# Performance work log

Hardware: AMD Instinct MI355X
Metric: run time of the kernel (lower is better)

The kernel has to match this reference:

```python
import jax, jax.numpy as jnp
import numpy as np

T, A, E, N, W, HID, FD = 4096, 1024, 512, 32768, 10, 150, 20
GI = 2 * A + E  # 2560
BINS = jnp.array([1, 2, 3, 4, 8, 16, 32, 64], dtype=jnp.int32)


def _mlp(x, W1, b1, W2, b2, W3, b3):
    # Score module: Linear->ReLU->Linear->ReLU->Linear->1 (dropout is a no-op in eval)
    h = jax.nn.relu(x @ W1 + b1)
    h = jax.nn.relu(h @ W2 + b2)
    return h @ W3 + b3


def setup_inputs() -> dict:
    key = jax.random.key(0)
    ks = jax.random.split(key, 20)
    s = 0.02
    inp = {
        "states": jax.random.normal(ks[0], (T, A), jnp.float32),
        "embeds": jax.random.normal(ks[1], (T, E), jnp.float32),
        "span_starts": jax.random.randint(ks[2], (N,), 0, T - W, jnp.int32),
        "span_widths": jax.random.randint(ks[3], (N,), 1, W + 1, jnp.int32),
        # attention Score params (input A)
        "Wa1": jax.random.normal(ks[4], (A, HID)) * s, "ba1": jnp.zeros((HID,)),
        "Wa2": jax.random.normal(ks[5], (HID, HID)) * s, "ba2": jnp.zeros((HID,)),
        "Wa3": jax.random.normal(ks[6], (HID, 1)) * s, "ba3": jnp.zeros((1,)),
        # width Feature embedding table: len(bins)+1 = 9 rows
        "width_emb": jax.random.normal(ks[7], (9, FD)) * s,
        # mention Score params (input GI + FD)
        "Ws1": jax.random.normal(ks[8], (GI + FD, HID)) * s, "bs1": jnp.zeros((HID,)),
        "Ws2": jax.random.normal(ks[9], (HID, HID)) * s, "bs2": jnp.zeros((HID,)),
        "Ws3": jax.random.normal(ks[10], (HID, 1)) * s, "bs3": jnp.zeros((1,)),
    }
    return inp


def reference(states, embeds, span_starts, span_widths,
              Wa1, ba1, Wa2, ba2, Wa3, ba3, width_emb,
              Ws1, bs1, Ws2, bs2, Ws3, bs3):
    # per-token attention logits  [T]
    attns = _mlp(states, Wa1, ba1, Wa2, ba2, Wa3, ba3).squeeze(-1)
    offs = jnp.arange(W)                                   # [W]
    pos = span_starts[:, None] + offs[None, :]             # [N, W]
    mask = offs[None, :] < span_widths[:, None]            # ragged span mask
    pos_c = jnp.clip(pos, 0, T - 1)
    logit = jnp.where(mask, attns[pos_c], -jnp.inf)        # [N, W]
    w = jax.nn.softmax(logit, axis=1)                      # per-span softmax
    attn_sum = jnp.einsum('nw,nwe->ne', w, embeds[pos_c])  # [N, E]
    ends = span_starts + span_widths - 1
    bin_idx = jnp.sum(span_widths[:, None] >= BINS[None, :], axis=1)
    size = width_emb[bin_idx]                              # [N, FD]
    g = jnp.concatenate([states[span_starts], states[ends], attn_sum, size], axis=1)
    scores = _mlp(g, Ws1, bs1, Ws2, bs2, Ws3, bs3).squeeze(-1)  # [N]
    return scores
```

## Files before the change

kernel.cpp:

```cpp
#include <hip/hip_runtime.h>
#include <math.h>

#define T_TOK 4096
#define A_DIM 1024
#define E_DIM 512
#define N_SPAN 32768
#define W_MAX 10
#define HID 150
#define FD 20

#define PR  160
#define KP2 160

#define WS_ATTNS 0
#define WS_PB    4096
#define WS_WPACK 1314816
#define WS_SB    1627856
#define WS_EB    3725008
#define PB_P0 0
#define PB_P1 655360
#define PB_P2 1310720
#define PB_P3 1966080
#define WP_ST  0
#define WP_V   491520
#define WP_A2  573440
#define WP_S2  599040
#define WP_WE1 624640
#define WP_TOTAL 626080
#define SB_PIECES 524288
#define EB_PIECES 262144
#define PK_ITEMS (WP_TOTAL + SB_PIECES + EB_PIECES)

typedef short  bf16x8 __attribute__((ext_vector_type(8)));
typedef float  f32x4  __attribute__((ext_vector_type(4)));

__device__ __forceinline__ float4 ld4(const float* p) { return *(const float4*)p; }

__device__ __forceinline__ unsigned short f2bf(float f) {
    unsigned u = __float_as_uint(f);
    unsigned r = u + 0x7fffu + ((u >> 16) & 1u);
    return (unsigned short)(r >> 16);
}
__device__ __forceinline__ float bf2f(short s) {
    return __uint_as_float(((unsigned)(unsigned short)s) << 16);
}
__device__ __forceinline__ bf16x8 cvt_frag(const float* p) {
    float4 u = ld4(p), v = ld4(p + 4);
    bf16x8 f;
    f[0] = (short)f2bf(u.x); f[1] = (short)f2bf(u.y);
    f[2] = (short)f2bf(u.z); f[3] = (short)f2bf(u.w);
    f[4] = (short)f2bf(v.x); f[5] = (short)f2bf(v.y);
    f[6] = (short)f2bf(v.z); f[7] = (short)f2bf(v.w);
    return f;
}

typedef const __attribute__((address_space(1))) unsigned int as1_u32;
typedef __attribute__((address_space(3))) unsigned int as3_u32;
__device__ __forceinline__ void dma16(const void* g, void* l) {
    __builtin_amdgcn_global_load_lds((as1_u32*)g, (as3_u32*)l, 16, 0, 0);
}
template<int N> __device__ __forceinline__ void waitv() {
    asm volatile("s_waitcnt vmcnt(%0)" :: "n"(N) : "memory");
}

__global__ __launch_bounds__(256) void prepack_kernel(
    const float* __restrict__ states, const float* __restrict__ embeds,
    const float* __restrict__ Wa1, const float* __restrict__ Ws1,
    const float* __restrict__ Wa2, const float* __restrict__ Ws2,
    const float* __restrict__ width_emb,
    unsigned short* __restrict__ wp, unsigned short* __restrict__ Sb,
    unsigned short* __restrict__ Eb)
{
    int idx = blockIdx.x * 256 + threadIdx.x;
    if (idx >= PK_ITEMS) return;
    if (idx < WP_TOTAL) {
        float v = 0.f;
        if (idx < WP_V) {
            int gidx = idx / 163840, r = idx % 163840;
            int ngrp = r / 81920, r2 = r % 81920;
            int c = r2 / 2560, d = r2 % 2560;
            int n = d >> 5, qsw = (d >> 3) & 3, off = d & 7;
            int q = qsw ^ ((n >> 1) & 3);
            int k = c * 32 + q * 8 + off;
            int gn = ngrp * 80 + n;
            const float* W = (gidx == 0) ? Wa1 : Ws1 + (size_t)(gidx - 1) * 1024 * HID;
            if (gn < HID) v = W[(size_t)k * HID + gn];
        } else if (idx < WP_A2) {
            int r = idx - WP_V;
            int ngrp = r / 40960, r2 = r % 40960;
            int c = r2 / 2560, d = r2 % 2560;
            int n = d >> 5, qsw = (d >> 3) & 3, off = d & 7;
            int q = qsw ^ ((n >> 1) & 3);
            int k = c * 32 + q * 8 + off;
            int gn = ngrp * 80 + n;
            if (gn < HID) v = Ws1[(size_t)(2048 + k) * HID + gn];
        } else if (idx < WP_S2) {
            int e = idx - WP_A2;
            int n = e / KP2, k = e % KP2;
            if (n < HID && k < HID) v = Wa2[(size_t)k * HID + n];
        } else if (idx < WP_WE1) {
            int e = idx - WP_S2;
            int n = e / KP2, k = e % KP2;
            if (n < HID && k < HID) v = Ws2[(size_t)k * HID + n];
        } else {
            int e = idx - WP_WE1;
            int b = e / KP2, n = e % KP2;
            if (n < HID)
                for (int k = 0; k < FD; ++k)
                    v = fmaf(width_emb[b * FD + k], Ws1[(size_t)(2560 + k) * HID + n], v);
        }
        wp[idx] = f2bf(v);
    } else if (idx < WP_TOTAL + SB_PIECES) {
        int p = idx - WP_TOTAL;
        int mb = p >> 11, r = p & 2047;
        int c = r >> 6, d8 = r & 63;
        int m = d8 >> 2, qsw = d8 & 3;
        int q = qsw ^ ((m >> 1) & 3);
        const float* src = states + (size_t)(mb * 16 + m) * A_DIM + c * 32 + q * 8;
        *(bf16x8*)(Sb + (size_t)p * 8) = cvt_frag(src);
    } else {
        int p = idx - WP_TOTAL - SB_PIECES;
        int mb = p >> 10, r = p & 1023;
        int c = r >> 6, d8 = r & 63;
        int m = d8 >> 2, qsw = d8 & 3;
        int q = qsw ^ ((m >> 1) & 3);
        const float* src = embeds + (size_t)(mb * 16 + m) * E_DIM + c * 32 + q * 8;
        *(bf16x8*)(Eb + (size_t)p * 8) = cvt_frag(src);
    }
}

template<int NC>
__device__ __forceinline__ void gemm_dma(
    const unsigned short* __restrict__ srcA, const unsigned short* __restrict__ srcB,
    unsigned short (*__restrict__ bufB)[2560], unsigned short (*__restrict__ bufA)[512],
    int lane, int l15, int quad, f32x4 (&acc)[5])
{
    const int swz = (quad ^ ((l15 >> 1) & 3)) * 8;
    const int bl = l15 * 32 + swz;
#define DMAC(c) { _Pragma("unroll")                                          \
        for (int i = 0; i < 5; ++i)                                          \
            dma16(srcB + (size_t)(c) * 2560 + i * 512 + lane * 8,            \
                  &bufB[(c) % 3][i * 512]);                                  \
        dma16(srcA + (size_t)(c) * 512 + lane * 8, &bufA[(c) % 3][0]); }
    DMAC(0);
    DMAC(1);
#pragma unroll
    for (int c = 0; c < NC; ++c) {
        if (c + 2 < NC) DMAC(c + 2);
        if (c + 2 < NC)      waitv<12>();
        else if (c + 1 < NC) waitv<6>();
        else                 waitv<0>();
        bf16x8 af = *(const bf16x8*)(&bufA[c % 3][0] + bl);
        const unsigned short* bb = &bufB[c % 3][0];
#pragma unroll
        for (int t = 0; t < 5; ++t) {
            bf16x8 bf = *(const bf16x8*)(bb + t * 512 + bl);
            acc[t] = __builtin_amdgcn_mfma_f32_16x16x32_bf16(af, bf, acc[t], 0, 0, 0);
        }
    }
#undef DMAC
}

__global__ __launch_bounds__(64) void token_kernel(
    const unsigned short* __restrict__ Sb, const unsigned short* __restrict__ Eb,
    const unsigned short* __restrict__ wp, unsigned short* __restrict__ Pb)
{
    __shared__ __align__(16) unsigned short bufB[3][2560];
    __shared__ __align__(16) unsigned short bufA[3][512];

    const int lane = threadIdx.x, l15 = lane & 15, quad = lane >> 4;
    const int task = blockIdx.x;

    f32x4 acc[5];
#pragma unroll
    for (int t = 0; t < 5; ++t)
#pragma unroll
        for (int i = 0; i < 4; ++i) acc[t][i] = 0.f;

    int m0, gidx, ngrp;
    if (task < 1536) {
        const int mb = task / 6;
        m0 = mb * 16;
        const int sub = task % 6;
        gidx = sub >> 1;
        ngrp = sub & 1;
        const unsigned short* srcA = Sb + (size_t)mb * 16384;
        const unsigned short* srcB = wp + WP_ST + gidx * 163840 + ngrp * 81920;
        gemm_dma<32>(srcA, srcB, bufB, bufA, lane, l15, quad, acc);
    } else {
        const int e = task - 1536;
        const int mb = e >> 1;
        m0 = mb * 16;
        ngrp = e & 1;
        gidx = 3;
        const unsigned short* srcA = Eb + (size_t)mb * 8192;
        const unsigned short* srcB = wp + WP_V + ngrp * 40960;
        gemm_dma<16>(srcA, srcB, bufB, bufA, lane, l15, quad, acc);
    }

    unsigned short* Pg = Pb + (size_t)gidx * 655360;
#pragma unroll
    for (int t = 0; t < 5; ++t) {
        const int col = ngrp * 80 + t * 16 + l15;
#pragma unroll
        for (int i = 0; i < 4; ++i)
            Pg[(size_t)(m0 + quad * 4 + i) * PR + col] =
                (col < HID) ? f2bf(acc[t][i]) : (unsigned short)0;
    }
}

__global__ __launch_bounds__(64) void attn_tail_kernel(
    const unsigned short* __restrict__ P0, const float* __restrict__ ba1,
    const unsigned short* __restrict__ wp, const float* __restrict__ ba2,
    const float* __restrict__ Wa3, const float* __restrict__ ba3,
    float* __restrict__ attns)
{
    const int t0 = blockIdx.x * 16;
    const int lane = threadIdx.x, l15 = lane & 15, quad = lane >> 4;

    f32x4 acc[10];
#pragma unroll
    for (int nt = 0; nt < 10; ++nt)
#pragma unroll
        for (int i = 0; i < 4; ++i) acc[nt][i] = 0.f;

    const unsigned short* prow = P0 + (size_t)(t0 + l15) * PR;
    const unsigned short* bb = wp + WP_A2 + l15 * KP2 + quad * 8;

#pragma unroll
    for (int c = 0; c < 5; ++c) {
        const int k0 = c * 32;
        const int kk = k0 + quad * 8;
        bf16x8 raw = *(const bf16x8*)(prow + kk);
        bf16x8 af;
#pragma unroll
        for (int j = 0; j < 8; ++j) {
            const float b = (kk + j < HID) ? ba1[kk + j] : 0.f;
            af[j] = (short)f2bf(fmaxf(bf2f(raw[j]) + b, 0.f));
        }
#pragma unroll
        for (int nt = 0; nt < 10; ++nt) {
            bf16x8 bf = *(const bf16x8*)(bb + nt * 16 * KP2 + k0);
            acc[nt] = __builtin_amdgcn_mfma_f32_16x16x32_bf16(af, bf, acc[nt], 0, 0, 0);
        }
    }

    float sc[4] = {0.f, 0.f, 0.f, 0.f};
#pragma unroll
    for (int nt = 0; nt < 10; ++nt) {
        const int col = nt * 16 + l15;
        const float w3 = (col < HID) ? Wa3[col] : 0.f;
        const float b2 = (col < HID) ? ba2[col] : 0.f;
#pragma unroll
        for (int i = 0; i < 4; ++i)
            sc[i] = fmaf(fmaxf(acc[nt][i] + b2, 0.f), w3, sc[i]);
    }
#pragma unroll
    for (int off = 8; off >= 1; off >>= 1)
#pragma unroll
        for (int i = 0; i < 4; ++i) sc[i] += __shfl_down(sc[i], off, 16);
    if (l15 == 0) {
        const float b3 = ba3[0];
#pragma unroll
        for (int i = 0; i < 4; ++i) attns[t0 + quad * 4 + i] = sc[i] + b3;
    }
}

__global__ __launch_bounds__(256) void span_kernel(
    const unsigned short* __restrict__ Pb, const float* __restrict__ attns,
    const unsigned short* __restrict__ wp,
    const int* __restrict__ span_starts, const int* __restrict__ span_widths,
    const float* __restrict__ bs1, const float* __restrict__ bs2,
    const float* __restrict__ Ws3, const float* __restrict__ bs3,
    float* __restrict__ out)
{
    __shared__ unsigned short sHb[32][168];
    __shared__ float s_wgt[32][W_MAX];
    __shared__ int s_st[32], s_wd[32], s_bin[32];
    __shared__ float sPart[4][32];
    __shared__ float sb1[KP2];

    const int tid = threadIdx.x;
    const int n0s = blockIdx.x * 32;

    if (tid < KP2) sb1[tid] = (tid < HID) ? bs1[tid] : 0.f;
    if (tid < 32) {
        int st = span_starts[n0s + tid], wd = span_widths[n0s + tid];
        s_st[tid] = st; s_wd[tid] = wd;
        s_bin[tid] = (wd >= 1) + (wd >= 2) + (wd >= 3) + (wd >= 4) +
                     (wd >= 8) + (wd >= 16) + (wd >= 32) + (wd >= 64);
        float lg[W_MAX];
        float m = -1e30f;
#pragma unroll
        for (int w = 0; w < W_MAX; ++w)
            if (w < wd) { float a = attns[st + w]; lg[w] = a; m = fmaxf(m, a); }
        float sum = 0.f;
#pragma unroll
        for (int w = 0; w < W_MAX; ++w) {
            float e = (w < wd) ? __expf(lg[w] - m) : 0.f;
            lg[w] = e; sum += e;
        }
        float inv = 1.f / sum;
#pragma unroll
        for (int w = 0; w < W_MAX; ++w) s_wgt[tid][w] = lg[w] * inv;
    }
    __syncthreads();

    {
        const unsigned short* P1b = Pb + PB_P1;
        const unsigned short* P2b = Pb + PB_P2;
        const unsigned short* P3b = Pb + PB_P3;
        const unsigned short* WEb = wp + WP_WE1;
        const int s = tid >> 3, jl = tid & 7;
        const int st = s_st[s], wd = s_wd[s];
        const size_t rs = (size_t)st * PR;
        const size_t re = (size_t)(st + wd - 1) * PR;
        const size_t rb = (size_t)s_bin[s] * PR;
        for (int c = jl; c < 20; c += 8) {
            const int j = c * 8;
            bf16x8 u1 = *(const bf16x8*)(P1b + rs + j);
            bf16x8 u2 = *(const bf16x8*)(P2b + re + j);
            bf16x8 uw = *(const bf16x8*)(WEb + rb + j);
            float acc[8];
#pragma unroll
            for (int i = 0; i < 8; ++i)
                acc[i] = bf2f(u1[i]) + bf2f(u2[i]) + bf2f(uw[i]) + sb1[j + i];
#pragma unroll
            for (int w = 0; w < W_MAX; ++w) {
                if (w < wd) {
                    float wt = s_wgt[s][w];
                    bf16x8 uv = *(const bf16x8*)(P3b + rs + (size_t)w * PR + j);
#pragma unroll
                    for (int i = 0; i < 8; ++i)
                        acc[i] = fmaf(wt, bf2f(uv[i]), acc[i]);
                }
            }
            bf16x8 pk;
#pragma unroll
            for (int i = 0; i < 8; ++i) pk[i] = (short)f2bf(fmaxf(acc[i], 0.f));
            *(bf16x8*)&sHb[s][j] = pk;
        }
    }
    __syncthreads();

    const int wv = tid >> 6, lane = tid & 63, l15 = lane & 15, quad = lane >> 4;
    const int nb = (wv < 2) ? wv * 3 : 6 + (wv - 2) * 2;
    const int cnt = (wv < 2) ? 3 : 2;

    f32x4 a2[2][3];
#pragma unroll
    for (int mt = 0; mt < 2; ++mt)
#pragma unroll
        for (int t = 0; t < 3; ++t)
#pragma unroll
            for (int i = 0; i < 4; ++i) a2[mt][t][i] = 0.f;

#pragma unroll
    for (int c = 0; c < 5; ++c) {
        int k0 = c * 32;
        bf16x8 af0 = *(const bf16x8*)&sHb[l15][k0 + quad * 8];
        bf16x8 af1 = *(const bf16x8*)&sHb[16 + l15][k0 + quad * 8];
#pragma unroll
        for (int t = 0; t < 3; ++t) {
            if (t < cnt) {
                bf16x8 b = *(const bf16x8*)(wp + WP_S2 +
                            (size_t)((nb + t) * 16 + l15) * KP2 + k0 + quad * 8);
                a2[0][t] = __builtin_amdgcn_mfma_f32_16x16x32_bf16(af0, b, a2[0][t], 0, 0, 0);
                a2[1][t] = __builtin_amdgcn_mfma_f32_16x16x32_bf16(af1, b, a2[1][t], 0, 0, 0);
            }
        }
    }

    float sc[2][4];
#pragma unroll
    for (int mt = 0; mt < 2; ++mt)
#pragma unroll
        for (int i = 0; i < 4; ++i) sc[mt][i] = 0.f;
#pragma unroll
    for (int t = 0; t < 3; ++t) {
        if (t < cnt) {
            int col = (nb + t) * 16 + l15;
            float w3 = (col < HID) ? Ws3[col] : 0.f;
            float b2 = (col < HID) ? bs2[col] : 0.f;
#pragma unroll
            for (int mt = 0; mt < 2; ++mt)
#pragma unroll
                for (int i = 0; i < 4; ++i)
                    sc[mt][i] = fmaf(fmaxf(a2[mt][t][i] + b2, 0.f), w3, sc[mt][i]);
        }
    }
#pragma unroll
    for (int off = 8; off >= 1; off >>= 1)
#pragma unroll
        for (int mt = 0; mt < 2; ++mt)
#pragma unroll
            for (int i = 0; i < 4; ++i)
                sc[mt][i] += __shfl_down(sc[mt][i], off, 16);
    if (l15 == 0) {
#pragma unroll
        for (int mt = 0; mt < 2; ++mt)
#pragma unroll
            for (int i = 0; i < 4; ++i)
                sPart[wv][mt * 16 + quad * 4 + i] = sc[mt][i];
    }
    __syncthreads();
    if (tid < 32)
        out[n0s + tid] = sPart[0][tid] + sPart[1][tid] + sPart[2][tid] +
                         sPart[3][tid] + bs3[0];
}

extern "C" void kernel_launch(void* const* d_in, const int* in_sizes, int n_in,
                              void* d_out, int out_size, void* d_ws, size_t ws_size,
                              hipStream_t stream)
{
    const float* states      = (const float*)d_in[0];
    const float* embeds      = (const float*)d_in[1];
    const int*   span_starts = (const int*)d_in[2];
    const int*   span_widths = (const int*)d_in[3];
    const float* Wa1 = (const float*)d_in[4];
    const float* ba1 = (const float*)d_in[5];
    const float* Wa2 = (const float*)d_in[6];
    const float* ba2 = (const float*)d_in[7];
    const float* Wa3 = (const float*)d_in[8];
    const float* ba3 = (const float*)d_in[9];
    const float* width_emb = (const float*)d_in[10];
    const float* Ws1 = (const float*)d_in[11];
    const float* bs1 = (const float*)d_in[12];
    const float* Ws2 = (const float*)d_in[13];
    const float* bs2 = (const float*)d_in[14];
    const float* Ws3 = (const float*)d_in[15];
    const float* bs3 = (const float*)d_in[16];
    float* out = (float*)d_out;

    float* ws    = (float*)d_ws;
    float* attns = ws + WS_ATTNS;
    unsigned short* Pb    = (unsigned short*)(ws + WS_PB);
    unsigned short* wpack = (unsigned short*)(ws + WS_WPACK);
    unsigned short* Sb    = (unsigned short*)(ws + WS_SB);
    unsigned short* Eb    = (unsigned short*)(ws + WS_EB);

    hipLaunchKernelGGL(prepack_kernel, dim3((PK_ITEMS + 255) / 256), dim3(256), 0, stream,
                       states, embeds, Wa1, Ws1, Wa2, Ws2, width_emb,
                       wpack, Sb, Eb);
    hipLaunchKernelGGL(token_kernel, dim3(2048), dim3(64), 0, stream,
                       Sb, Eb, wpack, Pb);
    hipLaunchKernelGGL(attn_tail_kernel, dim3(T_TOK / 16), dim3(64), 0, stream,
                       Pb + PB_P0, ba1, wpack, ba2, Wa3, ba3, attns);
    hipLaunchKernelGGL(span_kernel, dim3(N_SPAN / 32), dim3(256), 0, stream,
                       Pb, attns, wpack, span_starts, span_widths,
                       bs1, bs2, Ws3, bs3, out);
}
```

Baseline: 146.4 us.

## Fuse attention MLP tail into token GEMM and sort spans by width

The token kernel now runs two waves per block, one per N-group, so each block computes all 160 output columns for a 16-row tile. For the attention projection (gidx 0), the first-layer result is kept in LDS and the second and third MLP layers are done in place, which removes the separate attn_tail kernel and the P0 round trip through global memory. The span kernel also ranks the 32 spans in each block by width, so neighbouring threads in the gather loop see similar trip counts and diverge less. Outputs are scattered back to their original indices. The costs are extra LDS per block, added block syncs, and an O(32) rank computation per span.

```diff
diff --git a/kernel.cpp b/kernel.cpp
--- a/kernel.cpp
+++ b/kernel.cpp
@@ -161,15 +161,21 @@
 #undef DMAC
 }
 
-__global__ __launch_bounds__(64) void token_kernel(
+__global__ __launch_bounds__(128) void token_kernel(
     const unsigned short* __restrict__ Sb, const unsigned short* __restrict__ Eb,
-    const unsigned short* __restrict__ wp, unsigned short* __restrict__ Pb)
+    const unsigned short* __restrict__ wp, unsigned short* __restrict__ Pb,
+    const float* __restrict__ ba1, const float* __restrict__ ba2,
+    const float* __restrict__ Wa3, const float* __restrict__ ba3,
+    float* __restrict__ attns)
 {
-    __shared__ __align__(16) unsigned short bufB[3][2560];
-    __shared__ __align__(16) unsigned short bufA[3][512];
-
-    const int lane = threadIdx.x, l15 = lane & 15, quad = lane >> 4;
+    __shared__ __align__(16) unsigned short bufB[2][3][2560];
+    __shared__ __align__(16) unsigned short bufA[2][3][512];
+    __shared__ float sPartA[2][16];
+
+    const int wv = threadIdx.x >> 6;
+    const int lane = threadIdx.x & 63, l15 = lane & 15, quad = lane >> 4;
     const int task = blockIdx.x;
+    const int ngrp = wv;
 
     f32x4 acc[5];
 #pragma unroll
@@ -177,92 +183,83 @@
 #pragma unroll
         for (int i = 0; i < 4; ++i) acc[t][i] = 0.f;
 
-    int m0, gidx, ngrp;
-    if (task < 1536) {
-        const int mb = task / 6;
+    int m0, gidx;
+    if (task < 768) {
+        const int mb = task / 3;
         m0 = mb * 16;
-        const int sub = task % 6;
-        gidx = sub >> 1;
-        ngrp = sub & 1;
+        gidx = task % 3;
         const unsigned short* srcA = Sb + (size_t)mb * 16384;
         const unsigned short* srcB = wp + WP_ST + gidx * 163840 + ngrp * 81920;
-        gemm_dma<32>(srcA, srcB, bufB, bufA, lane, l15, quad, acc);
+        gemm_dma<32>(srcA, srcB, bufB[wv], bufA[wv], lane, l15, quad, acc);
     } else {
-        const int e = task - 1536;
-        const int mb = e >> 1;
+        const int mb = task - 768;
         m0 = mb * 16;
-        ngrp = e & 1;
         gidx = 3;
         const unsigned short* srcA = Eb + (size_t)mb * 8192;
         const unsigned short* srcB = wp + WP_V + ngrp * 40960;
-        gemm_dma<16>(srcA, srcB, bufB, bufA, lane, l15, quad, acc);
-    }
-
-    unsigned short* Pg = Pb + (size_t)gidx * 655360;
-#pragma unroll
-    for (int t = 0; t < 5; ++t) {
-        const int col = ngrp * 80 + t * 16 + l15;
-#pragma unroll
-        for (int i = 0; i < 4; ++i)
-            Pg[(size_t)(m0 + quad * 4 + i) * PR + col] =
-                (col < HID) ? f2bf(acc[t][i]) : (unsigned short)0;
-    }
-}
-
-__global__ __launch_bounds__(64) void attn_tail_kernel(
-    const unsigned short* __restrict__ P0, const float* __restrict__ ba1,
-    const unsigned short* __restrict__ wp, const float* __restrict__ ba2,
-    const float* __restrict__ Wa3, const float* __restrict__ ba3,
-    float* __restrict__ attns)
-{
-    const int t0 = blockIdx.x * 16;
-    const int lane = threadIdx.x, l15 = lane & 15, quad = lane >> 4;
-
-    f32x4 acc[10];
-#pragma unroll
-    for (int nt = 0; nt < 10; ++nt)
-#pragma unroll
-        for (int i = 0; i < 4; ++i) acc[nt][i] = 0.f;
-
-    const unsigned short* prow = P0 + (size_t)(t0 + l15) * PR;
-    const unsigned short* bb = wp + WP_A2 + l15 * KP2 + quad * 8;
-
-#pragma unroll
-    for (int c = 0; c < 5; ++c) {
-        const int k0 = c * 32;
-        const int kk = k0 + quad * 8;
-        bf16x8 raw = *(const bf16x8*)(prow + kk);
-        bf16x8 af;
-#pragma unroll
-        for (int j = 0; j < 8; ++j) {
-            const float b = (kk + j < HID) ? ba1[kk + j] : 0.f;
-            af[j] = (short)f2bf(fmaxf(bf2f(raw[j]) + b, 0.f));
-        }
-#pragma unroll
-        for (int nt = 0; nt < 10; ++nt) {
-            bf16x8 bf = *(const bf16x8*)(bb + nt * 16 * KP2 + k0);
-            acc[nt] = __builtin_amdgcn_mfma_f32_16x16x32_bf16(af, bf, acc[nt], 0, 0, 0);
-        }
-    }
-
-    float sc[4] = {0.f, 0.f, 0.f, 0.f};
-#pragma unroll
-    for (int nt = 0; nt < 10; ++nt) {
-        const int col = nt * 16 + l15;
-        const float w3 = (col < HID) ? Wa3[col] : 0.f;
-        const float b2 = (col < HID) ? ba2[col] : 0.f;
-#pragma unroll
-        for (int i = 0; i < 4; ++i)
-            sc[i] = fmaf(fmaxf(acc[nt][i] + b2, 0.f), w3, sc[i]);
-    }
-#pragma unroll
-    for (int off = 8; off >= 1; off >>= 1)
-#pragma unroll
-        for (int i = 0; i < 4; ++i) sc[i] += __shfl_down(sc[i], off, 16);
-    if (l15 == 0) {
-        const float b3 = ba3[0];
-#pragma unroll
-        for (int i = 0; i < 4; ++i) attns[t0 + quad * 4 + i] = sc[i] + b3;
+        gemm_dma<16>(srcA, srcB, bufB[wv], bufA[wv], lane, l15, quad, acc);
+    }
+
+    if (gidx == 0) {
+        unsigned short (*sHb)[168] = (unsigned short (*)[168])&bufB[0][0][0];
+        __syncthreads();
+#pragma unroll
+        for (int t = 0; t < 5; ++t) {
+            const int col = ngrp * 80 + t * 16 + l15;
+            const float b1 = (col < HID) ? ba1[col] : 0.f;
+#pragma unroll
+            for (int i = 0; i < 4; ++i)
+                sHb[quad * 4 + i][col] = f2bf(fmaxf(acc[t][i] + b1, 0.f));
+        }
+        __syncthreads();
+        f32x4 a2[5];
+#pragma unroll
+        for (int t = 0; t < 5; ++t)
+#pragma unroll
+            for (int i = 0; i < 4; ++i) a2[t][i] = 0.f;
+#pragma unroll
+        for (int c = 0; c < 5; ++c) {
+            const int kq = c * 32 + quad * 8;
+            bf16x8 af = *(const bf16x8*)&sHb[l15][kq];
+#pragma unroll
+            for (int t = 0; t < 5; ++t) {
+                const int nt = ngrp * 5 + t;
+                bf16x8 bf = *(const bf16x8*)(wp + WP_A2 +
+                            (size_t)(nt * 16 + l15) * KP2 + kq);
+                a2[t] = __builtin_amdgcn_mfma_f32_16x16x32_bf16(af, bf, a2[t], 0, 0, 0);
+            }
+        }
+        float sc[4] = {0.f, 0.f, 0.f, 0.f};
+#pragma unroll
+        for (int t = 0; t < 5; ++t) {
+            const int col = (ngrp * 5 + t) * 16 + l15;
+            const float w3 = (col < HID) ? Wa3[col] : 0.f;
+            const float b2 = (col < HID) ? ba2[col] : 0.f;
+#pragma unroll
+            for (int i = 0; i < 4; ++i)
+                sc[i] = fmaf(fmaxf(a2[t][i] + b2, 0.f), w3, sc[i]);
+        }
+#pragma unroll
+        for (int off = 8; off >= 1; off >>= 1)
+#pragma unroll
+            for (int i = 0; i < 4; ++i) sc[i] += __shfl_down(sc[i], off, 16);
+        if (l15 == 0)
+#pragma unroll
+            for (int i = 0; i < 4; ++i) sPartA[ngrp][quad * 4 + i] = sc[i];
+        __syncthreads();
+        if (threadIdx.x < 16)
+            attns[m0 + threadIdx.x] =
+                sPartA[0][threadIdx.x] + sPartA[1][threadIdx.x] + ba3[0];
+    } else {
+        unsigned short* Pg = Pb + (size_t)gidx * 655360;
+#pragma unroll
+        for (int t = 0; t < 5; ++t) {
+            const int col = ngrp * 80 + t * 16 + l15;
+#pragma unroll
+            for (int i = 0; i < 4; ++i)
+                Pg[(size_t)(m0 + quad * 4 + i) * PR + col] =
+                    (col < HID) ? f2bf(acc[t][i]) : (unsigned short)0;
+        }
     }
 }
 
@@ -276,7 +273,7 @@
 {
     __shared__ unsigned short sHb[32][168];
     __shared__ float s_wgt[32][W_MAX];
-    __shared__ int s_st[32], s_wd[32], s_bin[32];
+    __shared__ int s_st[32], s_wd[32], s_bin[32], s_oid[32], s_wdr[32];
     __shared__ float sPart[4][32];
     __shared__ float sb1[KP2];
 
@@ -284,11 +281,23 @@
     const int n0s = blockIdx.x * 32;
 
     if (tid < KP2) sb1[tid] = (tid < HID) ? bs1[tid] : 0.f;
+    int st = 0, wd = 0;
     if (tid < 32) {
-        int st = span_starts[n0s + tid], wd = span_widths[n0s + tid];
-        s_st[tid] = st; s_wd[tid] = wd;
-        s_bin[tid] = (wd >= 1) + (wd >= 2) + (wd >= 3) + (wd >= 4) +
-                     (wd >= 8) + (wd >= 16) + (wd >= 32) + (wd >= 64);
+        st = span_starts[n0s + tid];
+        wd = span_widths[n0s + tid];
+        s_wdr[tid] = wd;
+    }
+    __syncthreads();
+    if (tid < 32) {
+        int rank = 0;
+#pragma unroll
+        for (int j = 0; j < 32; ++j) {
+            const int wj = s_wdr[j];
+            rank += (wj < wd) || (wj == wd && j < tid);
+        }
+        s_st[rank] = st; s_wd[rank] = wd; s_oid[rank] = tid;
+        s_bin[rank] = (wd >= 1) + (wd >= 2) + (wd >= 3) + (wd >= 4) +
+                      (wd >= 8) + (wd >= 16) + (wd >= 32) + (wd >= 64);
         float lg[W_MAX];
         float m = -1e30f;
 #pragma unroll
@@ -302,7 +311,7 @@
         }
         float inv = 1.f / sum;
 #pragma unroll
-        for (int w = 0; w < W_MAX; ++w) s_wgt[tid][w] = lg[w] * inv;
+        for (int w = 0; w < W_MAX; ++w) s_wgt[rank][w] = lg[w] * inv;
     }
     __syncthreads();
 
@@ -312,9 +321,9 @@
         const unsigned short* P3b = Pb + PB_P3;
         const unsigned short* WEb = wp + WP_WE1;
         const int s = tid >> 3, jl = tid & 7;
-        const int st = s_st[s], wd = s_wd[s];
-        const size_t rs = (size_t)st * PR;
-        const size_t re = (size_t)(st + wd - 1) * PR;
+        const int sst = s_st[s], swd = s_wd[s];
+        const size_t rs = (size_t)sst * PR;
+        const size_t re = (size_t)(sst + swd - 1) * PR;
         const size_t rb = (size_t)s_bin[s] * PR;
         for (int c = jl; c < 20; c += 8) {
             const int j = c * 8;
@@ -327,7 +336,7 @@
                 acc[i] = bf2f(u1[i]) + bf2f(u2[i]) + bf2f(uw[i]) + sb1[j + i];
 #pragma unroll
             for (int w = 0; w < W_MAX; ++w) {
-                if (w < wd) {
+                if (w < swd) {
                     float wt = s_wgt[s][w];
                     bf16x8 uv = *(const bf16x8*)(P3b + rs + (size_t)w * PR + j);
 #pragma unroll
@@ -405,8 +414,8 @@
     }
     __syncthreads();
     if (tid < 32)
-        out[n0s + tid] = sPart[0][tid] + sPart[1][tid] + sPart[2][tid] +
-                         sPart[3][tid] + bs3[0];
+        out[n0s + s_oid[tid]] = sPart[0][tid] + sPart[1][tid] + sPart[2][tid] +
+                                sPart[3][tid] + bs3[0];
 }
 
 extern "C" void kernel_launch(void* const* d_in, const int* in_sizes, int n_in,
@@ -442,10 +451,8 @@
     hipLaunchKernelGGL(prepack_kernel, dim3((PK_ITEMS + 255) / 256), dim3(256), 0, stream,
                        states, embeds, Wa1, Ws1, Wa2, Ws2, width_emb,
                        wpack, Sb, Eb);
-    hipLaunchKernelGGL(token_kernel, dim3(2048), dim3(64), 0, stream,
-                       Sb, Eb, wpack, Pb);
-    hipLaunchKernelGGL(attn_tail_kernel, dim3(T_TOK / 16), dim3(64), 0, stream,
-                       Pb + PB_P0, ba1, wpack, ba2, Wa3, ba3, attns);
+    hipLaunchKernelGGL(token_kernel, dim3(1024), dim3(128), 0, stream,
+                       Sb, Eb, wpack, Pb, ba1, ba2, Wa3, ba3, attns);
     hipLaunchKernelGGL(span_kernel, dim3(N_SPAN / 32), dim3(256), 0, stream,
                        Pb, attns, wpack, span_starts, span_widths,
                        bs1, bs2, Ws3, bs3, out);
```

Measured after the change: 139.9 us. 4.5% less time.

## Deepen token GEMM DMA pipeline to four stages and sort spans by width

Applied to the files above, without the earlier changes.

The token GEMM's LDS ring buffer grows from three to four stages, so three chunks are kept in flight and the wait counts are adjusted to match. In the span kernel, the 32 spans of each block are ranked by width and stored in sorted order, with the original index kept so outputs are scattered back correctly. Each group of 8 threads handles one span, so sorting places spans of similar width in the same wavefront and is meant to reduce divergence in the per-width loop. The cost is more LDS per token block, which may lower occupancy, plus an extra barrier and an O(32) rank computation per span.

```diff
diff --git a/kernel.cpp b/kernel.cpp
--- a/kernel.cpp
+++ b/kernel.cpp
@@ -140,18 +140,20 @@
 #define DMAC(c) { _Pragma("unroll")                                          \
         for (int i = 0; i < 5; ++i)                                          \
             dma16(srcB + (size_t)(c) * 2560 + i * 512 + lane * 8,            \
-                  &bufB[(c) % 3][i * 512]);                                  \
-        dma16(srcA + (size_t)(c) * 512 + lane * 8, &bufA[(c) % 3][0]); }
+                  &bufB[(c) & 3][i * 512]);                                  \
+        dma16(srcA + (size_t)(c) * 512 + lane * 8, &bufA[(c) & 3][0]); }
     DMAC(0);
     DMAC(1);
+    DMAC(2);
 #pragma unroll
     for (int c = 0; c < NC; ++c) {
-        if (c + 2 < NC) DMAC(c + 2);
-        if (c + 2 < NC)      waitv<12>();
+        if (c + 3 < NC) DMAC(c + 3);
+        if (c + 3 < NC)      waitv<18>();
+        else if (c + 2 < NC) waitv<12>();
         else if (c + 1 < NC) waitv<6>();
         else                 waitv<0>();
-        bf16x8 af = *(const bf16x8*)(&bufA[c % 3][0] + bl);
-        const unsigned short* bb = &bufB[c % 3][0];
+        bf16x8 af = *(const bf16x8*)(&bufA[c & 3][0] + bl);
+        const unsigned short* bb = &bufB[c & 3][0];
 #pragma unroll
         for (int t = 0; t < 5; ++t) {
             bf16x8 bf = *(const bf16x8*)(bb + t * 512 + bl);
@@ -165,8 +167,8 @@
     const unsigned short* __restrict__ Sb, const unsigned short* __restrict__ Eb,
     const unsigned short* __restrict__ wp, unsigned short* __restrict__ Pb)
 {
-    __shared__ __align__(16) unsigned short bufB[3][2560];
-    __shared__ __align__(16) unsigned short bufA[3][512];
+    __shared__ __align__(16) unsigned short bufB[4][2560];
+    __shared__ __align__(16) unsigned short bufA[4][512];
 
     const int lane = threadIdx.x, l15 = lane & 15, quad = lane >> 4;
     const int task = blockIdx.x;
@@ -276,7 +278,7 @@
 {
     __shared__ unsigned short sHb[32][168];
     __shared__ float s_wgt[32][W_MAX];
-    __shared__ int s_st[32], s_wd[32], s_bin[32];
+    __shared__ int s_st[32], s_wd[32], s_bin[32], s_oid[32], s_wdr[32];
     __shared__ float sPart[4][32];
     __shared__ float sb1[KP2];
 
@@ -284,11 +286,23 @@
     const int n0s = blockIdx.x * 32;
 
     if (tid < KP2) sb1[tid] = (tid < HID) ? bs1[tid] : 0.f;
+    int st = 0, wd = 0;
     if (tid < 32) {
-        int st = span_starts[n0s + tid], wd = span_widths[n0s + tid];
-        s_st[tid] = st; s_wd[tid] = wd;
-        s_bin[tid] = (wd >= 1) + (wd >= 2) + (wd >= 3) + (wd >= 4) +
-                     (wd >= 8) + (wd >= 16) + (wd >= 32) + (wd >= 64);
+        st = span_starts[n0s + tid];
+        wd = span_widths[n0s + tid];
+        s_wdr[tid] = wd;
+    }
+    __syncthreads();
+    if (tid < 32) {
+        int rank = 0;
+#pragma unroll
+        for (int j = 0; j < 32; ++j) {
+            const int wj = s_wdr[j];
+            rank += (wj < wd) || (wj == wd && j < tid);
+        }
+        s_st[rank] = st; s_wd[rank] = wd; s_oid[rank] = tid;
+        s_bin[rank] = (wd >= 1) + (wd >= 2) + (wd >= 3) + (wd >= 4) +
+                      (wd >= 8) + (wd >= 16) + (wd >= 32) + (wd >= 64);
         float lg[W_MAX];
         float m = -1e30f;
 #pragma unroll
@@ -302,7 +316,7 @@
         }
         float inv = 1.f / sum;
 #pragma unroll
-        for (int w = 0; w < W_MAX; ++w) s_wgt[tid][w] = lg[w] * inv;
+        for (int w = 0; w < W_MAX; ++w) s_wgt[rank][w] = lg[w] * inv;
     }
     __syncthreads();
 
@@ -312,9 +326,9 @@
         const unsigned short* P3b = Pb + PB_P3;
         const unsigned short* WEb = wp + WP_WE1;
         const int s = tid >> 3, jl = tid & 7;
-        const int st = s_st[s], wd = s_wd[s];
-        const size_t rs = (size_t)st * PR;
-        const size_t re = (size_t)(st + wd - 1) * PR;
+        const int sst = s_st[s], swd = s_wd[s];
+        const size_t rs = (size_t)sst * PR;
+        const size_t re = (size_t)(sst + swd - 1) * PR;
         const size_t rb = (size_t)s_bin[s] * PR;
         for (int c = jl; c < 20; c += 8) {
             const int j = c * 8;
@@ -327,7 +341,7 @@
                 acc[i] = bf2f(u1[i]) + bf2f(u2[i]) + bf2f(uw[i]) + sb1[j + i];
 #pragma unroll
             for (int w = 0; w < W_MAX; ++w) {
-                if (w < wd) {
+                if (w < swd) {
                     float wt = s_wgt[s][w];
                     bf16x8 uv = *(const bf16x8*)(P3b + rs + (size_t)w * PR + j);
 #pragma unroll
@@ -405,8 +419,8 @@
     }
     __syncthreads();
     if (tid < 32)
-        out[n0s + tid] = sPart[0][tid] + sPart[1][tid] + sPart[2][tid] +
-                         sPart[3][tid] + bs3[0];
+        out[n0s + s_oid[tid]] = sPart[0][tid] + sPart[1][tid] + sPart[2][tid] +
+                                sPart[3][tid] + bs3[0];
 }
 
 extern "C" void kernel_launch(void* const* d_in, const int* in_sizes, int n_in,
```

Result: no change. 149.0 us (+1.8%).
